# Optimization experiments

Hardware: AMD Instinct MI355X
Metric: run time of the kernel (lower is better)

The kernel has to match this reference:

```python
import jax, jax.numpy as jnp
import numpy as np

N_NODES = 100000
N_GRAPHS = 512


def gcn_conv(x, W, b, src, dst, n_nodes):
    """PyG GCNConv: out = D^{-1/2} (A + I) D^{-1/2} (x W) + b, scatter at dst."""
    xw = x @ W  # [N, out_dim]
    # add self loops
    loop = jnp.arange(n_nodes, dtype=src.dtype)
    src_f = jnp.concatenate([src, loop])
    dst_f = jnp.concatenate([dst, loop])
    # symmetric normalization: deg from unit edge weights on dst
    deg = jax.ops.segment_sum(jnp.ones_like(dst_f, dtype=xw.dtype), dst_f,
                              num_segments=n_nodes)
    dinv = jnp.where(deg > 0, jax.lax.rsqrt(deg), 0.0)
    norm = dinv[src_f] * dinv[dst_f]  # [E+N]
    msg = xw[src_f] * norm[:, None]   # gather + scale, [E+N, out_dim]
    out = jax.ops.segment_sum(msg, dst_f, num_segments=n_nodes)
    return out + b


def global_mean_pool(x, batch, num_graphs):
    s = jax.ops.segment_sum(x, batch, num_segments=num_graphs)
    cnt = jax.ops.segment_sum(jnp.ones((x.shape[0],), x.dtype), batch,
                              num_segments=num_graphs)
    return s / jnp.maximum(cnt, 1.0)[:, None]


def setup_inputs() -> dict:
    key = jax.random.key(0)
    ks = jax.random.split(key, 10)
    d_in, h1, h2, d_out = 128, 128, 128, 32
    n_edges = 1600000
    x = jax.random.normal(ks[0], (N_NODES, d_in), dtype=jnp.float32)
    edge_index = jax.random.randint(ks[1], (2, n_edges), 0, N_NODES, dtype=jnp.int64)
    batch = jnp.sort(jax.random.randint(ks[2], (N_NODES,), 0, N_GRAPHS, dtype=jnp.int64))
    s1 = 1.0 / np.sqrt(d_in)
    s2 = 1.0 / np.sqrt(h1)
    s3 = 1.0 / np.sqrt(h2)
    W1 = jax.random.uniform(ks[3], (d_in, h1), jnp.float32, -s1, s1)
    b1 = jnp.zeros((h1,), jnp.float32)
    W2 = jax.random.uniform(ks[4], (h1, h2), jnp.float32, -s2, s2)
    b2 = jnp.zeros((h2,), jnp.float32)
    Wl = jax.random.uniform(ks[5], (h2, d_out), jnp.float32, -s3 * np.sqrt(6.0), s3 * np.sqrt(6.0))
    bl = jax.random.uniform(ks[6], (d_out,), jnp.float32, -s3, s3)
    return {"x": x, "edge_index": edge_index, "batch": batch,
            "W1": W1, "b1": b1, "W2": W2, "b2": b2, "Wl": Wl, "bl": bl}


def reference(x, edge_index, batch, W1, b1, W2, b2, Wl, bl):
    src, dst = edge_index[0], edge_index[1]
    h = gcn_conv(x, W1, b1, src, dst, N_NODES)
    h = jax.nn.relu(h)
    h = gcn_conv(h, W2, b2, src, dst, N_NODES)
    g = global_mean_pool(h, batch, N_GRAPHS)
    g = jax.nn.relu(g)
    return g @ Wl + bl
```

## Files before the change

kernel.cpp:

```cpp
#include <hip/hip_runtime.h>
#include <hip/hip_fp16.h>

#define DIM 128
#define NGRAPH 512
#define BUCKET_SHIFT 9
#define BUCKET_NODES 512

typedef _Float16 half8 __attribute__((ext_vector_type(8)));
typedef float floatx4 __attribute__((ext_vector_type(4)));

__device__ __forceinline__ int detect64(const int* __restrict__ ei) {
  int all0 = 1;
#pragma unroll
  for (int k = 0; k < 32; ++k) all0 &= (ei[2 * k + 1] == 0);
  return all0;
}

__device__ __forceinline__ int edge_at(const int* p, long long idx, int is64) {
  return is64 ? p[idx * 2] : p[(size_t)idx];
}

__global__ __launch_bounds__(256) void k_bucket_hist(const int* __restrict__ ei, int E,
                                                     int* __restrict__ bucket_count,
                                                     int nbuck) {
  __shared__ int h[256];
  int tid = threadIdx.x;
  h[tid] = 0;
  __syncthreads();
  int is64 = detect64(ei);
  int half = E >> 1;
  if (is64) {
    const int4* dp = (const int4*)(ei + 2 * (size_t)E);
    for (int t = blockIdx.x * 256 + tid; t < half; t += gridDim.x * 256) {
      int4 d = dp[t];
      atomicAdd(&h[d.x >> BUCKET_SHIFT], 1);
      atomicAdd(&h[d.z >> BUCKET_SHIFT], 1);
    }
  } else {
    const int2* dp = (const int2*)(ei + (size_t)E);
    for (int t = blockIdx.x * 256 + tid; t < half; t += gridDim.x * 256) {
      int2 d = dp[t];
      atomicAdd(&h[d.x >> BUCKET_SHIFT], 1);
      atomicAdd(&h[d.y >> BUCKET_SHIFT], 1);
    }
  }
  __syncthreads();
  if (tid < nbuck && h[tid]) atomicAdd(&bucket_count[tid], h[tid]);
  if ((E & 1) && blockIdx.x == 0 && tid == 0) {
    int d = edge_at(ei, (long long)E + (E - 1), is64);
    atomicAdd(&bucket_count[d >> BUCKET_SHIFT], 1);
  }
}

__global__ __launch_bounds__(256) void k_bucket_scan(const int* __restrict__ bucket_count,
                                                     int* __restrict__ bucket_off,
                                                     int* __restrict__ bucket_cursor,
                                                     int* __restrict__ row_off,
                                                     int nbuck, int N, int E) {
  __shared__ int s[256];
  int t = threadIdx.x;
  int v = (t < nbuck) ? bucket_count[t] : 0;
  s[t] = v;
  __syncthreads();
  for (int off = 1; off < 256; off <<= 1) {
    int u = (t >= off) ? s[t - off] : 0;
    __syncthreads();
    s[t] += u;
    __syncthreads();
  }
  int excl = s[t] - v;
  if (t < nbuck) { bucket_off[t] = excl; bucket_cursor[t] = excl; }
  if (t == 0) { bucket_off[nbuck] = E; row_off[N] = E; }
}

__global__ __launch_bounds__(256) void k_scatter(const int* __restrict__ ei, int E,
                                                 int* __restrict__ flag,
                                                 int* __restrict__ bucket_cursor,
                                                 int2* __restrict__ staging, int nbuck) {
  __shared__ int h[256];
  __shared__ int basebuf[256];
  int tid = threadIdx.x;
  int half = E >> 1;
  int ppb = (half + gridDim.x - 1) / gridDim.x;
  int lo = blockIdx.x * ppb;
  int hi = min(lo + ppb, half);
  h[tid] = 0;
  __syncthreads();
  int is64 = detect64(ei);
  if (blockIdx.x == 0 && tid == 0) *flag = is64;
  if (is64) {
    const int4* dp = (const int4*)(ei + 2 * (size_t)E);
    for (int t = lo + tid; t < hi; t += 256) {
      int4 d = dp[t];
      atomicAdd(&h[d.x >> BUCKET_SHIFT], 1);
      atomicAdd(&h[d.z >> BUCKET_SHIFT], 1);
    }
  } else {
    const int2* dp = (const int2*)(ei + (size_t)E);
    for (int t = lo + tid; t < hi; t += 256) {
      int2 d = dp[t];
      atomicAdd(&h[d.x >> BUCKET_SHIFT], 1);
      atomicAdd(&h[d.y >> BUCKET_SHIFT], 1);
    }
  }
  __syncthreads();
  if (tid < nbuck) {
    int c = h[tid];
    if (c) basebuf[tid] = atomicAdd(&bucket_cursor[tid], c);
    h[tid] = 0;
  }
  __syncthreads();
  if (is64) {
    const int4* sp = (const int4*)ei;
    const int4* dp = (const int4*)(ei + 2 * (size_t)E);
    for (int t = lo + tid; t < hi; t += 256) {
      int4 sv = sp[t];
      int4 dv = dp[t];
      int b0 = dv.x >> BUCKET_SHIFT;
      int l0 = atomicAdd(&h[b0], 1);
      staging[basebuf[b0] + l0] = make_int2(sv.x, dv.x);
      int b1 = dv.z >> BUCKET_SHIFT;
      int l1 = atomicAdd(&h[b1], 1);
      staging[basebuf[b1] + l1] = make_int2(sv.z, dv.z);
    }
  } else {
    const int2* sp = (const int2*)ei;
    const int2* dp = (const int2*)(ei + (size_t)E);
    for (int t = lo + tid; t < hi; t += 256) {
      int2 sv = sp[t];
      int2 dv = dp[t];
      int b0 = dv.x >> BUCKET_SHIFT;
      int l0 = atomicAdd(&h[b0], 1);
      staging[basebuf[b0] + l0] = make_int2(sv.x, dv.x);
      int b1 = dv.y >> BUCKET_SHIFT;
      int l1 = atomicAdd(&h[b1], 1);
      staging[basebuf[b1] + l1] = make_int2(sv.y, dv.y);
    }
  }
  if ((E & 1) && blockIdx.x == 0 && tid == 0) {
    int s0 = edge_at(ei, E - 1, is64);
    int d0 = edge_at(ei, (long long)E + (E - 1), is64);
    int pos = atomicAdd(&bucket_cursor[d0 >> BUCKET_SHIFT], 1);
    staging[pos] = make_int2(s0, d0);
  }
}

__global__ __launch_bounds__(256) void k_csr_build(const int2* __restrict__ staging,
                                                   const int* __restrict__ bucket_off,
                                                   int* __restrict__ row_off,
                                                   float* __restrict__ dinv,
                                                   int* __restrict__ csr_src, int N) {
  __shared__ int cnt_s[BUCKET_NODES];
  __shared__ int s[256];
  int tid = threadIdx.x;
  int b = blockIdx.x;
  int base = b << BUCKET_SHIFT;
  cnt_s[tid] = 0;
  cnt_s[tid + 256] = 0;
  __syncthreads();
  int start = bucket_off[b], end = bucket_off[b + 1];
  for (int i = start + tid; i < end; i += 256) {
    int2 e = staging[i];
    atomicAdd(&cnt_s[e.y - base], 1);
  }
  __syncthreads();
  int a0 = cnt_s[2 * tid], a1 = cnt_s[2 * tid + 1];
  int ps = a0 + a1;
  s[tid] = ps;
  __syncthreads();
  for (int off = 1; off < 256; off <<= 1) {
    int u = (tid >= off) ? s[tid - off] : 0;
    __syncthreads();
    s[tid] += u;
    __syncthreads();
  }
  int excl = s[tid] - ps;
  int r0 = start + excl;
  int r1 = r0 + a0;
  cnt_s[2 * tid] = r0;
  cnt_s[2 * tid + 1] = r1;
  int n0 = base + 2 * tid, n1 = n0 + 1;
  if (n0 < N) { row_off[n0] = r0; dinv[n0] = rsqrtf((float)(a0 + 1)); }
  if (n1 < N) { row_off[n1] = r1; dinv[n1] = rsqrtf((float)(a1 + 1)); }
  __syncthreads();
  for (int i = start + tid; i < end; i += 256) {
    int2 e = staging[i];
    int pos = atomicAdd(&cnt_s[e.y - base], 1);
    csr_src[pos] = e.x;
  }
}

__global__ __launch_bounds__(256) void k_gemm_mfma(
    const float* __restrict__ A, const float* __restrict__ W,
    const float* __restrict__ dinv, __half* __restrict__ Y, int M) {
  __shared__ _Float16 WH[16384];
  __shared__ _Float16 WL[16384];
  __shared__ _Float16 OT[4][16 * 128];
  int tid = threadIdx.x;

  for (int idx = tid; idx < 2048; idx += 256) {
    int l = idx & 63, c = (idx >> 6) & 7, s = idx >> 9;
    int kbase = s * 32 + ((l >> 4) << 3);
    int col = c * 16 + (l & 15);
#pragma unroll
    for (int j = 0; j < 8; ++j) {
      float w = W[(kbase + j) * 128 + col];
      _Float16 hh = (_Float16)w;
      WH[idx * 8 + j] = hh;
      WL[idx * 8 + j] = (_Float16)(w - (float)hh);
    }
  }
  __syncthreads();

  int wid = tid >> 6, l = tid & 63;
  int row0 = blockIdx.x * 64 + wid * 16;
  int arow = row0 + (l & 15);
  if (arow >= M) arow = M - 1;

  floatx4 acc[8];
#pragma unroll
  for (int c = 0; c < 8; ++c) acc[c] = (floatx4){0.f, 0.f, 0.f, 0.f};

#pragma unroll
  for (int s = 0; s < 4; ++s) {
    const float* ap = &A[(size_t)arow * 128 + s * 32 + ((l >> 4) << 3)];
    float4 f0 = *(const float4*)ap;
    float4 f1 = *(const float4*)(ap + 4);
    float fv[8] = {f0.x, f0.y, f0.z, f0.w, f1.x, f1.y, f1.z, f1.w};
    half8 ah, alo;
#pragma unroll
    for (int j = 0; j < 8; ++j) {
      _Float16 hh = (_Float16)fv[j];
      ah[j] = hh;
      alo[j] = (_Float16)(fv[j] - (float)hh);
    }
#pragma unroll
    for (int c = 0; c < 8; ++c) {
      int fi = ((s * 8 + c) * 64 + l) * 8;
      half8 bh = *(half8*)&WH[fi];
      half8 bl8 = *(half8*)&WL[fi];
      acc[c] = __builtin_amdgcn_mfma_f32_16x16x32_f16(ah, bh, acc[c], 0, 0, 0);
      acc[c] = __builtin_amdgcn_mfma_f32_16x16x32_f16(alo, bh, acc[c], 0, 0, 0);
      acc[c] = __builtin_amdgcn_mfma_f32_16x16x32_f16(ah, bl8, acc[c], 0, 0, 0);
    }
  }

  _Float16* ot = &OT[wid][0];
  int lrb = (l >> 4) * 4;
  float dv[4];
#pragma unroll
  for (int r = 0; r < 4; ++r) {
    int gr = row0 + lrb + r;
    dv[r] = (gr < M) ? dinv[gr] : 0.f;
  }
#pragma unroll
  for (int c = 0; c < 8; ++c)
#pragma unroll
    for (int r = 0; r < 4; ++r)
      ot[(lrb + r) * 128 + c * 16 + (l & 15)] = (_Float16)(acc[c][r] * dv[r]);
  const float4* otf = (const float4*)ot;
#pragma unroll
  for (int q = 0; q < 4; ++q) {
    int idx = q * 64 + l;
    int lrow = idx >> 4;
    int coff = (idx & 15) * 8;
    int grow = row0 + lrow;
    if (grow < M) *(float4*)&Y[(size_t)grow * 128 + coff] = otf[idx];
  }
}

__global__ __launch_bounds__(256) void k_aggregate(
    const __half* __restrict__ y, const int* __restrict__ csr_src,
    const int* __restrict__ row_off, const float* __restrict__ dinv,
    const float* __restrict__ bias, float* __restrict__ out, int do_relu, int N) {
  __shared__ int sidx[1024];
  int tid = threadIdx.x;
  int n0 = blockIdx.x * 4;
  int lastn = min(n0 + 4, N);
  int blockBeg = row_off[n0];
  int blockEnd = row_off[lastn];
  int len = blockEnd - blockBeg;
  int nload = min(len, 1024);
  for (int t = tid; t < nload; t += 256) sidx[t] = csr_src[blockBeg + t];
  __syncthreads();
  int node = n0 + (tid >> 6);
  if (node >= N) return;
  int lane = tid & 63;
  int beg = row_off[node], end = row_off[node + 1];
  float di = dinv[node];
  const __half2* base = (const __half2*)y;
  __half2 sv = base[(size_t)node * 64 + lane];
  float ax = __low2float(sv), ay = __high2float(sv);
  int e = beg;
  if (len <= nload) {
    for (; e + 8 <= end; e += 8) {
      int idx[8];
#pragma unroll
      for (int j = 0; j < 8; ++j) idx[j] = sidx[e - blockBeg + j];
      __half2 v[8];
#pragma unroll
      for (int j = 0; j < 8; ++j) v[j] = base[(size_t)idx[j] * 64 + lane];
#pragma unroll
      for (int j = 0; j < 8; ++j) { ax += __low2float(v[j]); ay += __high2float(v[j]); }
    }
    for (; e < end; ++e) {
      __half2 v0 = base[(size_t)sidx[e - blockBeg] * 64 + lane];
      ax += __low2float(v0); ay += __high2float(v0);
    }
  } else {
    for (; e < end; ++e) {
      __half2 v0 = base[(size_t)csr_src[e] * 64 + lane];
      ax += __low2float(v0); ay += __high2float(v0);
    }
  }
  float2 b = ((const float2*)bias)[lane];
  ax = di * ax + b.x;
  ay = di * ay + b.y;
  if (do_relu) { ax = fmaxf(ax, 0.f); ay = fmaxf(ay, 0.f); }
  float2 o; o.x = ax; o.y = ay;
  ((float2*)out)[(size_t)node * 64 + lane] = o;
}

__global__ __launch_bounds__(128) void k_pool_partial(
    const float* __restrict__ h, const int* __restrict__ batch,
    float* __restrict__ pooled, int* __restrict__ pcnt, int n,
    const int* __restrict__ flag) {
  __shared__ int sbatch[128];
  int tid = threadIdx.x;
  int n0 = blockIdx.x * 128;
  int n1 = min(n0 + 128, n);
  int cnt = n1 - n0;
  int is64 = *flag;
  if (tid < cnt) sbatch[tid] = is64 ? batch[2 * (n0 + tid)] : batch[n0 + tid];
  __syncthreads();
  float acc = 0.f;
  int gcur = sbatch[0];
  int runlen = 0;
  for (int r = 0; r < cnt; ++r) {
    int g = sbatch[r];
    if (g != gcur) {
      atomicAdd(&pooled[(size_t)gcur * 128 + tid], acc);
      if (tid == 0) atomicAdd(&pcnt[gcur], runlen);
      acc = 0.f; runlen = 0; gcur = g;
    }
    acc += h[(size_t)(n0 + r) * 128 + tid];
    ++runlen;
  }
  atomicAdd(&pooled[(size_t)gcur * 128 + tid], acc);
  if (tid == 0) atomicAdd(&pcnt[gcur], runlen);
}

__global__ __launch_bounds__(256) void k_final2(
    const float* __restrict__ pooled, const int* __restrict__ pcnt,
    const float* __restrict__ Wl, const float* __restrict__ bl,
    float* __restrict__ out) {
  __shared__ float sW[128 * 32];
  __shared__ float sg[8][128];
  int tid = threadIdx.x;
  for (int t = tid; t < 128 * 32; t += 256) sW[t] = Wl[t];
  int r = blockIdx.x * 8 + (tid >> 5);
  int c = tid & 31;
  float inv = 1.f / fmaxf((float)pcnt[r], 1.f);
#pragma unroll
  for (int q = 0; q < 4; ++q)
    sg[tid >> 5][c * 4 + q] = fmaxf(pooled[(size_t)r * 128 + c * 4 + q] * inv, 0.f);
  __syncthreads();
  const float* g = sg[tid >> 5];
  float acc = bl[c];
#pragma unroll 8
  for (int k = 0; k < 128; ++k) acc += g[k] * sW[k * 32 + c];
  out[r * 32 + c] = acc;
}

extern "C" void kernel_launch(void* const* d_in, const int* in_sizes, int n_in,
                              void* d_out, int out_size, void* d_ws, size_t ws_size,
                              hipStream_t stream) {
  const float* x   = (const float*)d_in[0];
  const int* ei    = (const int*)d_in[1];
  const int* batch = (const int*)d_in[2];
  const float* W1  = (const float*)d_in[3];
  const float* b1  = (const float*)d_in[4];
  const float* W2  = (const float*)d_in[5];
  const float* b2  = (const float*)d_in[6];
  const float* Wl  = (const float*)d_in[7];
  const float* bl  = (const float*)d_in[8];
  float* out = (float*)d_out;

  const int N = in_sizes[0] / DIM;
  const int E = in_sizes[1] / 2;
  const int NBUCK = (N + BUCKET_NODES - 1) >> BUCKET_SHIFT;

  size_t need = (size_t)N * DIM * 2 + (size_t)N * DIM * 4 + (size_t)E * 4
              + (size_t)(N + 1) * 4 + (size_t)N * 4 + 3 * 1088 + 64
              + (size_t)NGRAPH * DIM * 4 + NGRAPH * 4;
  if (ws_size < need) return;

  char* w = (char*)d_ws;
  __half* bufY  = (__half*)w; w += (size_t)N * DIM * 2;
  float* bufH   = (float*)w;  w += (size_t)N * DIM * 4;
  int* csr_src  = (int*)w;    w += (size_t)E * 4;
  int* row_off  = (int*)w;    w += (size_t)(N + 1) * 4;
  float* dinv   = (float*)w;  w += (size_t)N * 4;
  int* bucket_count  = (int*)w; w += 1088;
  int* bucket_off    = (int*)w; w += 1088;
  int* bucket_cursor = (int*)w; w += 1088;
  int* flag     = (int*)w;    w += 64;
  float* pooled = (float*)w;  w += (size_t)NGRAPH * DIM * 4;
  int* pcnt     = (int*)w;    w += NGRAPH * 4;
  int2* staging = (int2*)bufY;

  hipMemsetAsync(bucket_count, 0, 1088, stream);
  hipMemsetAsync(pooled, 0, (size_t)NGRAPH * DIM * 4 + NGRAPH * 4, stream);
  k_bucket_hist<<<1024, 256, 0, stream>>>(ei, E, bucket_count, NBUCK);
  k_bucket_scan<<<1, 256, 0, stream>>>(bucket_count, bucket_off, bucket_cursor,
                                       row_off, NBUCK, N, E);
  k_scatter<<<1024, 256, 0, stream>>>(ei, E, flag, bucket_cursor, staging, NBUCK);
  k_csr_build<<<NBUCK, 256, 0, stream>>>(staging, bucket_off, row_off, dinv, csr_src, N);

  k_gemm_mfma<<<(N + 63) / 64, 256, 0, stream>>>(x, W1, dinv, bufY, N);
  k_aggregate<<<(N + 3) / 4, 256, 0, stream>>>(bufY, csr_src, row_off, dinv, b1, bufH, 1, N);
  k_gemm_mfma<<<(N + 63) / 64, 256, 0, stream>>>(bufH, W2, dinv, bufY, N);
  k_aggregate<<<(N + 3) / 4, 256, 0, stream>>>(bufY, csr_src, row_off, dinv, b2, bufH, 0, N);
  k_pool_partial<<<(N + 127) / 128, 128, 0, stream>>>(bufH, batch, pooled, pcnt, N, flag);
  k_final2<<<NGRAPH / 8, 256, 0, stream>>>(pooled, pcnt, Wl, bl, out);
}
```

Measured before the change: 441.1 us.

## Store GEMM output in column-sliced layout and aggregate per slice for cache locality

The fp16 intermediate Y is now written as eight 16-column slices, each a contiguous [N,16] plane, and the output LDS tile is padded to reduce bank conflicts. Aggregation becomes slice-major: each block handles 128 nodes for one slice, and each thread pair gathers 16-byte vectors for one node. The goal is to keep each slice's working set (about 3.2MB) resident in L2/infinity cache during the random gathers, and to use wider per-thread loads. The trade-off is that CSR indices and row offsets are reloaded eight times, each thread handles a whole node's edge list (load imbalance), and the output stores are strided.

```diff
diff --git a/kernel.cpp b/kernel.cpp
--- a/kernel.cpp
+++ b/kernel.cpp
@@ -5,6 +5,8 @@
 #define NGRAPH 512
 #define BUCKET_SHIFT 9
 #define BUCKET_NODES 512
+#define AGG_NODES 128
+#define AGG_MAXE 4096
 
 typedef _Float16 half8 __attribute__((ext_vector_type(8)));
 typedef float floatx4 __attribute__((ext_vector_type(4)));
@@ -190,12 +192,13 @@
   }
 }
 
+#define OTS 136
 __global__ __launch_bounds__(256) void k_gemm_mfma(
     const float* __restrict__ A, const float* __restrict__ W,
-    const float* __restrict__ dinv, __half* __restrict__ Y, int M) {
+    const float* __restrict__ dinv, __half* __restrict__ Yb, int M) {
   __shared__ _Float16 WH[16384];
   __shared__ _Float16 WL[16384];
-  __shared__ _Float16 OT[4][16 * 128];
+  __shared__ _Float16 OT[4][16 * OTS];
   int tid = threadIdx.x;
 
   for (int idx = tid; idx < 2048; idx += 256) {
@@ -257,68 +260,92 @@
   for (int c = 0; c < 8; ++c)
 #pragma unroll
     for (int r = 0; r < 4; ++r)
-      ot[(lrb + r) * 128 + c * 16 + (l & 15)] = (_Float16)(acc[c][r] * dv[r]);
-  const float4* otf = (const float4*)ot;
+      ot[(lrb + r) * OTS + c * 16 + (l & 15)] = (_Float16)(acc[c][r] * dv[r]);
 #pragma unroll
   for (int q = 0; q < 4; ++q) {
     int idx = q * 64 + l;
-    int lrow = idx >> 4;
-    int coff = (idx & 15) * 8;
-    int grow = row0 + lrow;
-    if (grow < M) *(float4*)&Y[(size_t)grow * 128 + coff] = otf[idx];
+    int row = idx & 15;
+    int piece = idx >> 4;
+    int slice = piece >> 1, hp = piece & 1;
+    int grow = row0 + row;
+    float4 v = *(const float4*)&ot[row * OTS + piece * 8];
+    if (grow < M)
+      *(float4*)&Yb[((size_t)slice * M + grow) * 16 + hp * 8] = v;
   }
 }
 
 __global__ __launch_bounds__(256) void k_aggregate(
-    const __half* __restrict__ y, const int* __restrict__ csr_src,
+    const __half* __restrict__ Yb, const int* __restrict__ csr_src,
     const int* __restrict__ row_off, const float* __restrict__ dinv,
     const float* __restrict__ bias, float* __restrict__ out, int do_relu, int N) {
-  __shared__ int sidx[1024];
-  int tid = threadIdx.x;
-  int n0 = blockIdx.x * 4;
-  int lastn = min(n0 + 4, N);
-  int blockBeg = row_off[n0];
-  int blockEnd = row_off[lastn];
-  int len = blockEnd - blockBeg;
-  int nload = min(len, 1024);
+  __shared__ int sidx[AGG_MAXE];
+  __shared__ int srow[AGG_NODES + 1];
+  int tid = threadIdx.x;
+  int slice = blockIdx.x & 7;
+  int chunk = blockIdx.x >> 3;
+  int n0 = chunk * AGG_NODES;
+  if (tid <= AGG_NODES) srow[tid] = row_off[min(n0 + tid, N)];
+  __syncthreads();
+  int blockBeg = srow[0];
+  int len = srow[AGG_NODES] - blockBeg;
+  int nload = min(len, AGG_MAXE);
   for (int t = tid; t < nload; t += 256) sidx[t] = csr_src[blockBeg + t];
   __syncthreads();
-  int node = n0 + (tid >> 6);
+
+  int p = tid >> 1;
+  int plane = tid & 1;
+  int node = n0 + p;
   if (node >= N) return;
-  int lane = tid & 63;
-  int beg = row_off[node], end = row_off[node + 1];
+  int beg = srow[p] - blockBeg, end = srow[p + 1] - blockBeg;
+  const float4* ybase = (const float4*)(Yb + (size_t)slice * N * 16);
+  float a0 = 0.f, a1 = 0.f, a2 = 0.f, a3 = 0.f, a4 = 0.f, a5 = 0.f, a6 = 0.f, a7 = 0.f;
+#define ACC8(F4)                                                        \
+  {                                                                     \
+    float4 _f = (F4);                                                   \
+    __half2 _h0 = *(__half2*)&_f.x, _h1 = *(__half2*)&_f.y;             \
+    __half2 _h2 = *(__half2*)&_f.z, _h3 = *(__half2*)&_f.w;             \
+    a0 += __low2float(_h0); a1 += __high2float(_h0);                    \
+    a2 += __low2float(_h1); a3 += __high2float(_h1);                    \
+    a4 += __low2float(_h2); a5 += __high2float(_h2);                    \
+    a6 += __low2float(_h3); a7 += __high2float(_h3);                    \
+  }
+  int e = beg;
+  if (len <= AGG_MAXE) {
+    for (; e + 8 <= end; e += 8) {
+      int i0 = sidx[e + 0], i1 = sidx[e + 1], i2 = sidx[e + 2], i3 = sidx[e + 3];
+      int i4 = sidx[e + 4], i5 = sidx[e + 5], i6 = sidx[e + 6], i7 = sidx[e + 7];
+      float4 v0 = ybase[(size_t)i0 * 2 + plane];
+      float4 v1 = ybase[(size_t)i1 * 2 + plane];
+      float4 v2 = ybase[(size_t)i2 * 2 + plane];
+      float4 v3 = ybase[(size_t)i3 * 2 + plane];
+      float4 v4 = ybase[(size_t)i4 * 2 + plane];
+      float4 v5 = ybase[(size_t)i5 * 2 + plane];
+      float4 v6 = ybase[(size_t)i6 * 2 + plane];
+      float4 v7 = ybase[(size_t)i7 * 2 + plane];
+      ACC8(v0) ACC8(v1) ACC8(v2) ACC8(v3) ACC8(v4) ACC8(v5) ACC8(v6) ACC8(v7)
+    }
+    for (; e < end; ++e) ACC8(ybase[(size_t)sidx[e] * 2 + plane]);
+  } else {
+    for (; e < end; ++e) ACC8(ybase[(size_t)csr_src[blockBeg + e] * 2 + plane]);
+  }
+  ACC8(ybase[(size_t)node * 2 + plane]);
+#undef ACC8
   float di = dinv[node];
-  const __half2* base = (const __half2*)y;
-  __half2 sv = base[(size_t)node * 64 + lane];
-  float ax = __low2float(sv), ay = __high2float(sv);
-  int e = beg;
-  if (len <= nload) {
-    for (; e + 8 <= end; e += 8) {
-      int idx[8];
-#pragma unroll
-      for (int j = 0; j < 8; ++j) idx[j] = sidx[e - blockBeg + j];
-      __half2 v[8];
-#pragma unroll
-      for (int j = 0; j < 8; ++j) v[j] = base[(size_t)idx[j] * 64 + lane];
-#pragma unroll
-      for (int j = 0; j < 8; ++j) { ax += __low2float(v[j]); ay += __high2float(v[j]); }
-    }
-    for (; e < end; ++e) {
-      __half2 v0 = base[(size_t)sidx[e - blockBeg] * 64 + lane];
-      ax += __low2float(v0); ay += __high2float(v0);
-    }
-  } else {
-    for (; e < end; ++e) {
-      __half2 v0 = base[(size_t)csr_src[e] * 64 + lane];
-      ax += __low2float(v0); ay += __high2float(v0);
-    }
-  }
-  float2 b = ((const float2*)bias)[lane];
-  ax = di * ax + b.x;
-  ay = di * ay + b.y;
-  if (do_relu) { ax = fmaxf(ax, 0.f); ay = fmaxf(ay, 0.f); }
-  float2 o; o.x = ax; o.y = ay;
-  ((float2*)out)[(size_t)node * 64 + lane] = o;
+  const float* bp = &bias[slice * 16 + plane * 8];
+  float4 o0, o1;
+  o0.x = di * a0 + bp[0]; o0.y = di * a1 + bp[1];
+  o0.z = di * a2 + bp[2]; o0.w = di * a3 + bp[3];
+  o1.x = di * a4 + bp[4]; o1.y = di * a5 + bp[5];
+  o1.z = di * a6 + bp[6]; o1.w = di * a7 + bp[7];
+  if (do_relu) {
+    o0.x = fmaxf(o0.x, 0.f); o0.y = fmaxf(o0.y, 0.f);
+    o0.z = fmaxf(o0.z, 0.f); o0.w = fmaxf(o0.w, 0.f);
+    o1.x = fmaxf(o1.x, 0.f); o1.y = fmaxf(o1.y, 0.f);
+    o1.z = fmaxf(o1.z, 0.f); o1.w = fmaxf(o1.w, 0.f);
+  }
+  float* op = &out[(size_t)node * 128 + slice * 16 + plane * 8];
+  *(float4*)op = o0;
+  *(float4*)(op + 4) = o1;
 }
 
 __global__ __launch_bounds__(128) void k_pool_partial(
@@ -417,10 +444,11 @@
   k_scatter<<<1024, 256, 0, stream>>>(ei, E, flag, bucket_cursor, staging, NBUCK);
   k_csr_build<<<NBUCK, 256, 0, stream>>>(staging, bucket_off, row_off, dinv, csr_src, N);
 
+  int aggGrid = ((N + AGG_NODES - 1) / AGG_NODES) * 8;
   k_gemm_mfma<<<(N + 63) / 64, 256, 0, stream>>>(x, W1, dinv, bufY, N);
-  k_aggregate<<<(N + 3) / 4, 256, 0, stream>>>(bufY, csr_src, row_off, dinv, b1, bufH, 1, N);
+  k_aggregate<<<aggGrid, 256, 0, stream>>>(bufY, csr_src, row_off, dinv, b1, bufH, 1, N);
   k_gemm_mfma<<<(N + 63) / 64, 256, 0, stream>>>(bufH, W2, dinv, bufY, N);
-  k_aggregate<<<(N + 3) / 4, 256, 0, stream>>>(bufY, csr_src, row_off, dinv, b2, bufH, 0, N);
+  k_aggregate<<<aggGrid, 256, 0, stream>>>(bufY, csr_src, row_off, dinv, b2, bufH, 0, N);
   k_pool_partial<<<(N + 127) / 128, 128, 0, stream>>>(bufH, batch, pooled, pcnt, N, flag);
   k_final2<<<NGRAPH / 8, 256, 0, stream>>>(pooled, pcnt, Wl, bl, out);
 }
```

After: 485.1 us. 10.0% more time.

## Store hidden activations in fp16 and vectorize aggregation gathers to 16 bytes

Applied to the files above, without the earlier changes.

The aggregation output is now written as fp16 instead of fp32, so the second GEMM reads half the bytes. That GEMM is templated to take fp16 input directly, which skips the hi/lo split and one of its three MFMAs. The pooling kernel also reads fp16. The aggregation kernel is restructured so that 16-lane groups each gather a full 128-wide row with 16-byte loads, working on four edges at once and combining partial sums with cross-lane shuffles. The costs are lower precision in the hidden activations and extra shuffle reductions.

```diff
diff --git a/kernel.cpp b/kernel.cpp
--- a/kernel.cpp
+++ b/kernel.cpp
@@ -190,8 +190,9 @@
   }
 }
 
+template <int A16>
 __global__ __launch_bounds__(256) void k_gemm_mfma(
-    const float* __restrict__ A, const float* __restrict__ W,
+    const void* __restrict__ Av, const float* __restrict__ W,
     const float* __restrict__ dinv, __half* __restrict__ Y, int M) {
   __shared__ _Float16 WH[16384];
   __shared__ _Float16 WL[16384];
@@ -223,16 +224,22 @@
 
 #pragma unroll
   for (int s = 0; s < 4; ++s) {
-    const float* ap = &A[(size_t)arow * 128 + s * 32 + ((l >> 4) << 3)];
-    float4 f0 = *(const float4*)ap;
-    float4 f1 = *(const float4*)(ap + 4);
-    float fv[8] = {f0.x, f0.y, f0.z, f0.w, f1.x, f1.y, f1.z, f1.w};
     half8 ah, alo;
-#pragma unroll
-    for (int j = 0; j < 8; ++j) {
-      _Float16 hh = (_Float16)fv[j];
-      ah[j] = hh;
-      alo[j] = (_Float16)(fv[j] - (float)hh);
+    if (A16) {
+      const __half* A = (const __half*)Av;
+      ah = *(const half8*)&A[(size_t)arow * 128 + s * 32 + ((l >> 4) << 3)];
+    } else {
+      const float* A = (const float*)Av;
+      const float* ap = &A[(size_t)arow * 128 + s * 32 + ((l >> 4) << 3)];
+      float4 f0 = *(const float4*)ap;
+      float4 f1 = *(const float4*)(ap + 4);
+      float fv[8] = {f0.x, f0.y, f0.z, f0.w, f1.x, f1.y, f1.z, f1.w};
+#pragma unroll
+      for (int j = 0; j < 8; ++j) {
+        _Float16 hh = (_Float16)fv[j];
+        ah[j] = hh;
+        alo[j] = (_Float16)(fv[j] - (float)hh);
+      }
     }
 #pragma unroll
     for (int c = 0; c < 8; ++c) {
@@ -240,7 +247,8 @@
       half8 bh = *(half8*)&WH[fi];
       half8 bl8 = *(half8*)&WL[fi];
       acc[c] = __builtin_amdgcn_mfma_f32_16x16x32_f16(ah, bh, acc[c], 0, 0, 0);
-      acc[c] = __builtin_amdgcn_mfma_f32_16x16x32_f16(alo, bh, acc[c], 0, 0, 0);
+      if (!A16)
+        acc[c] = __builtin_amdgcn_mfma_f32_16x16x32_f16(alo, bh, acc[c], 0, 0, 0);
       acc[c] = __builtin_amdgcn_mfma_f32_16x16x32_f16(ah, bl8, acc[c], 0, 0, 0);
     }
   }
@@ -272,57 +280,84 @@
 __global__ __launch_bounds__(256) void k_aggregate(
     const __half* __restrict__ y, const int* __restrict__ csr_src,
     const int* __restrict__ row_off, const float* __restrict__ dinv,
-    const float* __restrict__ bias, float* __restrict__ out, int do_relu, int N) {
+    const float* __restrict__ bias, __half* __restrict__ out16, int do_relu, int N) {
   __shared__ int sidx[1024];
   int tid = threadIdx.x;
   int n0 = blockIdx.x * 4;
-  int lastn = min(n0 + 4, N);
   int blockBeg = row_off[n0];
-  int blockEnd = row_off[lastn];
+  int blockEnd = row_off[min(n0 + 4, N)];
   int len = blockEnd - blockBeg;
-  int nload = min(len, 1024);
+  bool staged = (len <= 1024);
+  int nload = staged ? len : 0;
   for (int t = tid; t < nload; t += 256) sidx[t] = csr_src[blockBeg + t];
   __syncthreads();
-  int node = n0 + (tid >> 6);
+
+  int wave = tid >> 6, l = tid & 63;
+  int node = n0 + wave;
   if (node >= N) return;
-  int lane = tid & 63;
+  int g = l >> 4, q = l & 15;
   int beg = row_off[node], end = row_off[node + 1];
-  float di = dinv[node];
-  const __half2* base = (const __half2*)y;
-  __half2 sv = base[(size_t)node * 64 + lane];
-  float ax = __low2float(sv), ay = __high2float(sv);
-  int e = beg;
-  if (len <= nload) {
-    for (; e + 8 <= end; e += 8) {
-      int idx[8];
-#pragma unroll
-      for (int j = 0; j < 8; ++j) idx[j] = sidx[e - blockBeg + j];
-      __half2 v[8];
-#pragma unroll
-      for (int j = 0; j < 8; ++j) v[j] = base[(size_t)idx[j] * 64 + lane];
-#pragma unroll
-      for (int j = 0; j < 8; ++j) { ax += __low2float(v[j]); ay += __high2float(v[j]); }
-    }
-    for (; e < end; ++e) {
-      __half2 v0 = base[(size_t)sidx[e - blockBeg] * 64 + lane];
-      ax += __low2float(v0); ay += __high2float(v0);
+
+  float a0 = 0.f, a1 = 0.f, a2 = 0.f, a3 = 0.f, a4 = 0.f, a5 = 0.f, a6 = 0.f, a7 = 0.f;
+#define ACC8(F4)                                                        \
+  {                                                                     \
+    float4 _f = (F4);                                                   \
+    __half2 _h0 = *(__half2*)&_f.x, _h1 = *(__half2*)&_f.y;             \
+    __half2 _h2 = *(__half2*)&_f.z, _h3 = *(__half2*)&_f.w;             \
+    a0 += __low2float(_h0); a1 += __high2float(_h0);                    \
+    a2 += __low2float(_h1); a3 += __high2float(_h1);                    \
+    a4 += __low2float(_h2); a5 += __high2float(_h2);                    \
+    a6 += __low2float(_h3); a7 += __high2float(_h3);                    \
+  }
+  if (g == 0) ACC8(*(const float4*)&y[(size_t)node * 128 + q * 8]);
+  if (staged) {
+    int rb = beg - blockBeg, re = end - blockBeg;
+#pragma unroll 2
+    for (int e = rb; e < re; e += 8) {
+      int e0 = e + g, e1 = e + 4 + g;
+      if (e0 < re) ACC8(*(const float4*)&y[(size_t)sidx[e0] * 128 + q * 8]);
+      if (e1 < re) ACC8(*(const float4*)&y[(size_t)sidx[e1] * 128 + q * 8]);
     }
   } else {
-    for (; e < end; ++e) {
-      __half2 v0 = base[(size_t)csr_src[e] * 64 + lane];
-      ax += __low2float(v0); ay += __high2float(v0);
-    }
-  }
-  float2 b = ((const float2*)bias)[lane];
-  ax = di * ax + b.x;
-  ay = di * ay + b.y;
-  if (do_relu) { ax = fmaxf(ax, 0.f); ay = fmaxf(ay, 0.f); }
-  float2 o; o.x = ax; o.y = ay;
-  ((float2*)out)[(size_t)node * 64 + lane] = o;
+    for (int e = beg; e < end; e += 8) {
+      int e0 = e + g, e1 = e + 4 + g;
+      if (e0 < end) ACC8(*(const float4*)&y[(size_t)csr_src[e0] * 128 + q * 8]);
+      if (e1 < end) ACC8(*(const float4*)&y[(size_t)csr_src[e1] * 128 + q * 8]);
+    }
+  }
+#undef ACC8
+  a0 += __shfl_xor(a0, 16); a1 += __shfl_xor(a1, 16);
+  a2 += __shfl_xor(a2, 16); a3 += __shfl_xor(a3, 16);
+  a4 += __shfl_xor(a4, 16); a5 += __shfl_xor(a5, 16);
+  a6 += __shfl_xor(a6, 16); a7 += __shfl_xor(a7, 16);
+  a0 += __shfl_xor(a0, 32); a1 += __shfl_xor(a1, 32);
+  a2 += __shfl_xor(a2, 32); a3 += __shfl_xor(a3, 32);
+  a4 += __shfl_xor(a4, 32); a5 += __shfl_xor(a5, 32);
+  a6 += __shfl_xor(a6, 32); a7 += __shfl_xor(a7, 32);
+
+  if (g == 0) {
+    float di = dinv[node];
+    const float* bp = &bias[q * 8];
+    float r0 = di * a0 + bp[0], r1 = di * a1 + bp[1];
+    float r2 = di * a2 + bp[2], r3 = di * a3 + bp[3];
+    float r4 = di * a4 + bp[4], r5 = di * a5 + bp[5];
+    float r6 = di * a6 + bp[6], r7 = di * a7 + bp[7];
+    if (do_relu) {
+      r0 = fmaxf(r0, 0.f); r1 = fmaxf(r1, 0.f); r2 = fmaxf(r2, 0.f);
+      r3 = fmaxf(r3, 0.f); r4 = fmaxf(r4, 0.f); r5 = fmaxf(r5, 0.f);
+      r6 = fmaxf(r6, 0.f); r7 = fmaxf(r7, 0.f);
+    }
+    __half2 h[4];
+    h[0] = __floats2half2_rn(r0, r1);
+    h[1] = __floats2half2_rn(r2, r3);
+    h[2] = __floats2half2_rn(r4, r5);
+    h[3] = __floats2half2_rn(r6, r7);
+    *(float4*)&out16[(size_t)node * 128 + q * 8] = *(float4*)h;
+  }
 }
 
 __global__ __launch_bounds__(128) void k_pool_partial(
-    const float* __restrict__ h, const int* __restrict__ batch,
+    const __half* __restrict__ h, const int* __restrict__ batch,
     float* __restrict__ pooled, int* __restrict__ pcnt, int n,
     const int* __restrict__ flag) {
   __shared__ int sbatch[128];
@@ -343,7 +378,7 @@
       if (tid == 0) atomicAdd(&pcnt[gcur], runlen);
       acc = 0.f; runlen = 0; gcur = g;
     }
-    acc += h[(size_t)(n0 + r) * 128 + tid];
+    acc += __half2float(h[(size_t)(n0 + r) * 128 + tid]);
     ++runlen;
   }
   atomicAdd(&pooled[(size_t)gcur * 128 + tid], acc);
@@ -396,8 +431,8 @@
   if (ws_size < need) return;
 
   char* w = (char*)d_ws;
-  __half* bufY  = (__half*)w; w += (size_t)N * DIM * 2;
-  float* bufH   = (float*)w;  w += (size_t)N * DIM * 4;
+  __half* bufY   = (__half*)w; w += (size_t)N * DIM * 2;
+  __half* bufH16 = (__half*)w; w += (size_t)N * DIM * 4;
   int* csr_src  = (int*)w;    w += (size_t)E * 4;
   int* row_off  = (int*)w;    w += (size_t)(N + 1) * 4;
   float* dinv   = (float*)w;  w += (size_t)N * 4;
@@ -417,10 +452,12 @@
   k_scatter<<<1024, 256, 0, stream>>>(ei, E, flag, bucket_cursor, staging, NBUCK);
   k_csr_build<<<NBUCK, 256, 0, stream>>>(staging, bucket_off, row_off, dinv, csr_src, N);
 
-  k_gemm_mfma<<<(N + 63) / 64, 256, 0, stream>>>(x, W1, dinv, bufY, N);
-  k_aggregate<<<(N + 3) / 4, 256, 0, stream>>>(bufY, csr_src, row_off, dinv, b1, bufH, 1, N);
-  k_gemm_mfma<<<(N + 63) / 64, 256, 0, stream>>>(bufH, W2, dinv, bufY, N);
-  k_aggregate<<<(N + 3) / 4, 256, 0, stream>>>(bufY, csr_src, row_off, dinv, b2, bufH, 0, N);
-  k_pool_partial<<<(N + 127) / 128, 128, 0, stream>>>(bufH, batch, pooled, pcnt, N, flag);
+  k_gemm_mfma<0><<<(N + 63) / 64, 256, 0, stream>>>(x, W1, dinv, bufY, N);
+  k_aggregate<<<(N + 3) / 4, 256, 0, stream>>>(bufY, csr_src, row_off, dinv, b1,
+                                               bufH16, 1, N);
+  k_gemm_mfma<1><<<(N + 63) / 64, 256, 0, stream>>>(bufH16, W2, dinv, bufY, N);
+  k_aggregate<<<(N + 3) / 4, 256, 0, stream>>>(bufY, csr_src, row_off, dinv, b2,
+                                               bufH16, 0, N);
+  k_pool_partial<<<(N + 127) / 128, 128, 0, stream>>>(bufH16, batch, pooled, pcnt, N, flag);
   k_final2<<<NGRAPH / 8, 256, 0, stream>>>(pooled, pcnt, Wl, bl, out);
 }
```

Measured after the change: 427.3 us. 1.03x faster.
